# Kernel optimization log

Hardware: AMD Instinct MI355X
Metric: run time of the kernel (lower is better)

The kernel has to match this reference:

```python
import jax, jax.numpy as jnp
import numpy as np

N = 100000        # nodes
E = 1600000       # edges (avg degree 16)
F = 128           # num_features
H = 8             # heads
D = F // H        # head_dim


def setup_inputs() -> dict:
    key = jax.random.key(0)
    ks = jax.random.split(key, 11)
    s = 1.0 / np.sqrt(F)
    return {
        "feat": jax.random.normal(ks[0], (N, F), dtype=jnp.float32),
        "edge_src": jax.random.randint(ks[1], (E,), 0, N, dtype=jnp.int32),
        "edge_dst": jax.random.randint(ks[2], (E,), 0, N, dtype=jnp.int32),
        "Wq": jax.random.uniform(ks[3], (F, F), jnp.float32, -s, s),
        "bq": jax.random.uniform(ks[4], (F,), jnp.float32, -s, s),
        "Wk": jax.random.uniform(ks[5], (F, F), jnp.float32, -s, s),
        "bk": jax.random.uniform(ks[6], (F,), jnp.float32, -s, s),
        "Wv": jax.random.uniform(ks[7], (F, F), jnp.float32, -s, s),
        "bv": jax.random.uniform(ks[8], (F,), jnp.float32, -s, s),
        "Wo": jax.random.uniform(ks[9], (F, F), jnp.float32, -s, s),
        "bo": jax.random.uniform(ks[10], (F,), jnp.float32, -s, s),
    }


def reference(feat, edge_src, edge_dst, Wq, bq, Wk, bk, Wv, bv, Wo, bo):
    scale = D ** -0.5
    # projections, split into heads: [N, H, D]
    q = ((feat @ Wq.T + bq) * scale).reshape(N, H, D)
    k = (feat @ Wk.T + bk).reshape(N, H, D)
    v = (feat @ Wv.T + bv).reshape(N, H, D)

    # per-edge dot product k[src] . q[dst] -> [E, H]  (dfn.u_dot_v)
    scores = jnp.einsum('ehd,ehd->eh', k[edge_src], q[edge_dst])

    # edge softmax normalized over incoming edges of each dst node
    m = jax.ops.segment_max(scores, edge_dst, num_segments=N)  # [N, H]
    m = jnp.where(jnp.isfinite(m), m, 0.0)
    e = jnp.exp(scores - m[edge_dst])                          # [E, H]
    z = jax.ops.segment_sum(e, edge_dst, num_segments=N)       # [N, H]
    alpha = e / z[edge_dst]                                    # [E, H]

    # weighted sum aggregation (u_mul_e + sum): [N, H, D]
    wv = alpha[:, :, None] * v[edge_src]                       # [E, H, D]
    attn = jax.ops.segment_sum(wv, edge_dst, num_segments=N)

    return attn.reshape(N, F) @ Wo.T + bo
```

## Files before the change

kernel.cpp:

```cpp
#include <hip/hip_runtime.h>
#include <math.h>

#define N_NODES 100000
#define N_EDGES 1600000
#define FDIM 128
#define NHEAD 8
#define HDIM 16
#define SCAT_PHASES 4

using bf16x8 = __attribute__((ext_vector_type(8))) short;
using half8  = __attribute__((ext_vector_type(8))) _Float16;
using half2t = __attribute__((ext_vector_type(2))) _Float16;
using f32x4  = __attribute__((ext_vector_type(4))) float;
using f32x2  = __attribute__((ext_vector_type(2))) float;

__device__ inline unsigned short f2bf(float f) {
    union { float f; unsigned int u; } x; x.f = f;
    unsigned int u = x.u;
    return (unsigned short)((u + 0x7fffu + ((u >> 16) & 1u)) >> 16);
}
__device__ inline unsigned short f2h(float f) {
    _Float16 h = (_Float16)f;
    return __builtin_bit_cast(unsigned short, h);
}
__device__ inline unsigned int packh2(float a, float b) {
    return (unsigned int)f2h(a) | ((unsigned int)f2h(b) << 16);
}
__device__ inline float h_lo(unsigned int u) {
    return (float)__builtin_bit_cast(_Float16, (unsigned short)(u & 0xffffu));
}
__device__ inline float h_hi(unsigned int u) {
    return (float)__builtin_bit_cast(_Float16, (unsigned short)(u >> 16));
}

#if __has_builtin(__builtin_amdgcn_cvt_pk_fp8_f32)
__device__ inline unsigned char fp8_enc(float x) {
    return (unsigned char)(__builtin_amdgcn_cvt_pk_fp8_f32(x, x, 0, false) & 0xff);
}
#else
__device__ inline unsigned char fp8_enc(float x) {
    unsigned int u = __builtin_bit_cast(unsigned int, x);
    unsigned int s = (u >> 24) & 0x80;
    float ax = fabsf(x);
    if (!(ax >= 0.001953125f)) {
        int m = (int)(ax * 512.f + 0.5f);
        return (unsigned char)(s | (unsigned)(m > 7 ? 7 : m));
    }
    if (ax > 448.f) return (unsigned char)(s | 0x7e);
    int e; float fr = frexpf(ax, &e);
    int q = (int)(fr * 16.f + 0.5f);
    if (q == 16) { q = 8; e += 1; }
    int exp = e - 1 + 7;
    if (exp <= 0) { int m = (int)(ax * 512.f + 0.5f); return (unsigned char)(s | (unsigned)(m > 7 ? 7 : m)); }
    if (exp > 15) return (unsigned char)(s | 0x7e);
    return (unsigned char)(s | (exp << 3) | (q & 7));
}
#endif

#if __has_builtin(__builtin_amdgcn_cvt_pk_f32_fp8)
#define FP8_HW_DECODE 1
#else
__device__ inline float fp8_dec_sw(unsigned char b) {
    int s = b >> 7, e = (b >> 3) & 15, m = b & 7;
    float v = (e == 0) ? ldexpf((float)m, -9) : ldexpf((float)(8 + m), e - 10);
    return s ? -v : v;
}
#endif

__device__ inline float dot_fp8_16(uint4 kr, const float* __restrict__ qq) {
    float s = 0.f;
#ifdef FP8_HW_DECODE
    f32x2 p;
    p = __builtin_amdgcn_cvt_pk_f32_fp8(kr.x, false); s = fmaf(p[0], qq[0],  s); s = fmaf(p[1], qq[1],  s);
    p = __builtin_amdgcn_cvt_pk_f32_fp8(kr.x, true);  s = fmaf(p[0], qq[2],  s); s = fmaf(p[1], qq[3],  s);
    p = __builtin_amdgcn_cvt_pk_f32_fp8(kr.y, false); s = fmaf(p[0], qq[4],  s); s = fmaf(p[1], qq[5],  s);
    p = __builtin_amdgcn_cvt_pk_f32_fp8(kr.y, true);  s = fmaf(p[0], qq[6],  s); s = fmaf(p[1], qq[7],  s);
    p = __builtin_amdgcn_cvt_pk_f32_fp8(kr.z, false); s = fmaf(p[0], qq[8],  s); s = fmaf(p[1], qq[9],  s);
    p = __builtin_amdgcn_cvt_pk_f32_fp8(kr.z, true);  s = fmaf(p[0], qq[10], s); s = fmaf(p[1], qq[11], s);
    p = __builtin_amdgcn_cvt_pk_f32_fp8(kr.w, false); s = fmaf(p[0], qq[12], s); s = fmaf(p[1], qq[13], s);
    p = __builtin_amdgcn_cvt_pk_f32_fp8(kr.w, true);  s = fmaf(p[0], qq[14], s); s = fmaf(p[1], qq[15], s);
#else
    unsigned int wds[4] = {kr.x, kr.y, kr.z, kr.w};
#pragma unroll
    for (int i = 0; i < 4; ++i)
#pragma unroll
        for (int j = 0; j < 4; ++j)
            s = fmaf(fp8_dec_sw((wds[i] >> (8 * j)) & 0xff), qq[i * 4 + j], s);
#endif
    return s;
}

__global__ __launch_bounds__(256) void convert_w_kernel(
    const float* __restrict__ W0, const float* __restrict__ W1,
    const float* __restrict__ W2, const float* __restrict__ W3,
    unsigned short* __restrict__ out)
{
    int i = blockIdx.x * 256 + threadIdx.x;
    int j  = i & 7;
    int l  = (i >> 3) & 63;
    int fk = i >> 9;
    int ks = fk & 3, nf = fk >> 2;
    int s = (nf * 16 + (l & 15)) * FDIM + ks * 32 + (l >> 4) * 8 + j;
    out[i]             = f2bf(W0[s]);
    out[16384 + i]     = f2bf(W1[s]);
    out[2 * 16384 + i] = f2bf(W2[s]);
    out[3 * 16384 + i] = f2h(W3[s]);
}

struct GemmArgs {
    const unsigned short* W[3];
    const float* b[3];
    void* out[3];
    float scale[3];
};

template<int NP, bool IN_F32, bool MFMA_F16, int OUTM>
__global__ __launch_bounds__(256, 2) void mfma_gemm_v2(
    const void* __restrict__ Ain, GemmArgs ga, int nrows)
{
    __shared__ unsigned short A_s[128][136];
    __shared__ unsigned short W_sh[8192];

    const int t  = threadIdx.x;
    const int r0 = blockIdx.x * 128;

#pragma unroll
    for (int it = 0; it < 8; ++it) {
        int i = t + it * 256;
        int r = i >> 4, c8 = (i & 15) << 3;
        int gr = r0 + r;
        if (IN_F32) {
            float4 v0 = make_float4(0.f, 0.f, 0.f, 0.f), v1 = v0;
            if (gr < nrows) {
                const float* Af = (const float*)Ain;
                v0 = *(const float4*)&Af[(size_t)gr * FDIM + c8];
                v1 = *(const float4*)&Af[(size_t)gr * FDIM + c8 + 4];
            }
            uint4 pk;
            pk.x = (unsigned)f2bf(v0.x) | ((unsigned)f2bf(v0.y) << 16);
            pk.y = (unsigned)f2bf(v0.z) | ((unsigned)f2bf(v0.w) << 16);
            pk.z = (unsigned)f2bf(v1.x) | ((unsigned)f2bf(v1.y) << 16);
            pk.w = (unsigned)f2bf(v1.z) | ((unsigned)f2bf(v1.w) << 16);
            *(uint4*)&A_s[r][c8] = pk;
        } else {
            uint4 v = make_uint4(0u, 0u, 0u, 0u);
            if (gr < nrows) {
                const unsigned short* Ab = (const unsigned short*)Ain;
                v = *(const uint4*)&Ab[(size_t)gr * FDIM + c8];
            }
            *(uint4*)&A_s[r][c8] = v;
        }
    }
    __syncthreads();

    const int w  = t >> 6, l = t & 63;
    const int lr = l & 15, lk = l >> 4;

    bf16x8 a[2][4];
#pragma unroll
    for (int rg = 0; rg < 2; ++rg)
#pragma unroll
        for (int ks = 0; ks < 4; ++ks)
            a[rg][ks] = *(const bf16x8*)&A_s[w * 32 + rg * 16 + lr][ks * 32 + lk * 8];

#pragma unroll
    for (int p = 0; p < NP; ++p) {
        const unsigned short* Wsrc = ga.W[p];
        f32x4 acc[2][8];
#pragma unroll
        for (int rg = 0; rg < 2; ++rg)
#pragma unroll
            for (int nf = 0; nf < 8; ++nf) acc[rg][nf] = (f32x4){0.f, 0.f, 0.f, 0.f};

#pragma unroll
        for (int h = 0; h < 2; ++h) {
#pragma unroll
            for (int it = 0; it < 4; ++it) {
                int chunk = t + it * 256;
                *(uint4*)&W_sh[chunk * 8] = *(const uint4*)&Wsrc[h * 8192 + chunk * 8];
            }
            __syncthreads();
#pragma unroll
            for (int nfl = 0; nfl < 4; ++nfl) {
                int nf = h * 4 + nfl;
#pragma unroll
                for (int ks = 0; ks < 4; ++ks) {
                    bf16x8 bfr = *(const bf16x8*)&W_sh[((nfl * 4 + ks) * 64 + l) * 8];
                    if (MFMA_F16) {
                        acc[0][nf] = __builtin_amdgcn_mfma_f32_16x16x32_f16(
                            __builtin_bit_cast(half8, a[0][ks]), __builtin_bit_cast(half8, bfr),
                            acc[0][nf], 0, 0, 0);
                        acc[1][nf] = __builtin_amdgcn_mfma_f32_16x16x32_f16(
                            __builtin_bit_cast(half8, a[1][ks]), __builtin_bit_cast(half8, bfr),
                            acc[1][nf], 0, 0, 0);
                    } else {
                        acc[0][nf] = __builtin_amdgcn_mfma_f32_16x16x32_bf16(a[0][ks], bfr, acc[0][nf], 0, 0, 0);
                        acc[1][nf] = __builtin_amdgcn_mfma_f32_16x16x32_bf16(a[1][ks], bfr, acc[1][nf], 0, 0, 0);
                    }
                }
            }
            __syncthreads();
        }

        const float* bias = ga.b[p];
        const float  scl  = ga.scale[p];
        const int    mode = (OUTM >> (2 * p)) & 3;

        if (mode == 0) {
            unsigned short* Oh = &A_s[0][0];
#pragma unroll
            for (int rg = 0; rg < 2; ++rg)
#pragma unroll
                for (int nf = 0; nf < 8; ++nf) {
                    int col = nf * 16 + lr;
                    float bv = bias[col];
#pragma unroll
                    for (int j = 0; j < 4; ++j)
                        Oh[(w * 32 + rg * 16 + lk * 4 + j) * 136 + col] = f2h((acc[rg][nf][j] + bv) * scl);
                }
            __syncthreads();
            unsigned short* outp = (unsigned short*)ga.out[p];
#pragma unroll
            for (int it = 0; it < 8; ++it) {
                int i = t + it * 256;
                int r = i >> 4, c8 = (i & 15) << 3;
                if (r0 + r < nrows)
                    *(uint4*)&outp[(size_t)(r0 + r) * FDIM + c8] = *(const uint4*)&Oh[r * 136 + c8];
            }
        } else if (mode == 1) {
            unsigned char* O8 = (unsigned char*)A_s;
#pragma unroll
            for (int rg = 0; rg < 2; ++rg)
#pragma unroll
                for (int nf = 0; nf < 8; ++nf) {
                    int col = nf * 16 + lr;
                    float bv = bias[col];
#pragma unroll
                    for (int j = 0; j < 4; ++j)
                        O8[(w * 32 + rg * 16 + lk * 4 + j) * 144 + col] = fp8_enc((acc[rg][nf][j] + bv) * scl);
                }
            __syncthreads();
            unsigned char* outp = (unsigned char*)ga.out[p];
#pragma unroll
            for (int it = 0; it < 4; ++it) {
                int i = t + it * 256;
                int r = i >> 3, c16 = (i & 7) << 4;
                if (r0 + r < nrows)
                    *(uint4*)&outp[(size_t)(r0 + r) * FDIM + c16] = *(const uint4*)&O8[r * 144 + c16];
            }
        } else {
            float* outp = (float*)ga.out[p];
#pragma unroll
            for (int rg = 0; rg < 2; ++rg)
#pragma unroll
                for (int nf = 0; nf < 8; ++nf) {
                    int col = nf * 16 + lr;
                    float bv = bias[col];
                    int row = r0 + w * 32 + rg * 16 + lk * 4;
#pragma unroll
                    for (int j = 0; j < 4; ++j)
                        if (row + j < nrows)
                            outp[(size_t)(row + j) * FDIM + col] = (acc[rg][nf][j] + bv) * scl;
                }
        }
    }
}

__global__ void count_rank_kernel(const int* __restrict__ dst, int* __restrict__ cnt,
                                  unsigned short* __restrict__ rank, int n)
{
    int i = blockIdx.x * 256 + threadIdx.x;
    if (i < n) {
        int d = __builtin_nontemporal_load(&dst[i]);
        rank[i] = (unsigned short)atomicAdd(&cnt[d], 1);
    }
}

__global__ void scan_a_kernel(const int* __restrict__ cnt, int* __restrict__ row_off,
                              int* __restrict__ part, int n)
{
    __shared__ int s[256];
    int t = threadIdx.x;
    int gid = blockIdx.x * 256 + t;
    int x = (gid < n) ? cnt[gid] : 0;
    s[t] = x;
    __syncthreads();
    for (int off = 1; off < 256; off <<= 1) {
        int val = (t >= off) ? s[t - off] : 0;
        __syncthreads();
        s[t] += val;
        __syncthreads();
    }
    if (gid < n) row_off[gid] = s[t] - x;
    if (t == 255) part[blockIdx.x] = s[255];
}

__global__ void scan_b_kernel(int* __restrict__ part, int nb)
{
    __shared__ int s[512];
    int t = threadIdx.x;
    int x = (t < nb) ? part[t] : 0;
    s[t] = x;
    __syncthreads();
    for (int off = 1; off < 512; off <<= 1) {
        int val = (t >= off) ? s[t - off] : 0;
        __syncthreads();
        s[t] += val;
        __syncthreads();
    }
    if (t < nb) part[t] = s[t] - x;
}

__global__ void scan_c_kernel(int* __restrict__ row_off, const int* __restrict__ part,
                              int n, int total)
{
    int gid = blockIdx.x * 256 + threadIdx.x;
    if (gid < n) row_off[gid] += part[blockIdx.x];
    if (gid == 0) row_off[n] = total;
}

__global__ void scatter_phase_kernel(const int* __restrict__ src, const int* __restrict__ dst,
                                     const unsigned short* __restrict__ rank,
                                     const int* __restrict__ row_off,
                                     int* __restrict__ csr_src, int n, int lo, int hi)
{
    int i = blockIdx.x * 256 + threadIdx.x;
    if (i < n) {
        int d = __builtin_nontemporal_load(&dst[i]);
        if (d >= lo && d < hi) {
            int pos = row_off[d] + (int)__builtin_nontemporal_load(&rank[i]);
            csr_src[pos] = __builtin_nontemporal_load(&src[i]);
        }
    }
}

__global__ __launch_bounds__(256) void attn_kernel(
    const unsigned short* __restrict__ q, const unsigned char* __restrict__ kf8,
    const unsigned short* __restrict__ v,
    const int* __restrict__ row_off, const int* __restrict__ csr_src,
    unsigned short* __restrict__ out, int nnodes)
{
    __shared__ float q_s[4][NHEAD][18];
    __shared__ float sc_s[4][64][NHEAD];
    __shared__ int   src_s[4][64];

    const int w = threadIdx.x >> 6;
    const int l = threadIdx.x & 63;
    const int node = blockIdx.x * 4 + w;
    if (node >= nnodes) return;

    {
        unsigned int qv = *(const unsigned int*)&q[(size_t)node * FDIM + l * 2];
        q_s[w][l >> 3][(l & 7) * 2]     = h_lo(qv);
        q_s[w][l >> 3][(l & 7) * 2 + 1] = h_hi(qv);
    }

    const int e_l  = l >> 3, h_sc = l & 7;
    const int h_ag = l >> 3, dp   = l & 7;
    const int vo   = h_ag * HDIM + dp * 2;

    const int start = row_off[node];
    const int end   = row_off[node + 1];

    float  m_run = -INFINITY;
    float  z_run = 0.f;
    float2 acc   = make_float2(0.f, 0.f);

    for (int c0 = start; c0 < end; c0 += 64) {
        const int cn = min(64, end - c0);

        for (int i = l; i < cn; i += 64)
            src_s[w][i] = csr_src[c0 + i];

        float cm = -INFINITY;
        const float* qq = &q_s[w][h_sc][0];
        for (int base = 0; base < cn; base += 32) {
            uint4 kr[4];
#pragma unroll
            for (int it = 0; it < 4; ++it) {
                int ei = base + it * 8 + e_l;
                if (ei < cn)
                    kr[it] = *(const uint4*)&kf8[(size_t)src_s[w][ei] * FDIM + h_sc * 16];
            }
#pragma unroll
            for (int it = 0; it < 4; ++it) {
                int ei = base + it * 8 + e_l;
                if (ei < cn) {
                    float s = dot_fp8_16(kr[it], qq);
                    sc_s[w][ei][h_sc] = s;
                    cm = fmaxf(cm, s);
                }
            }
        }
#pragma unroll
        for (int mask = 8; mask < 64; mask <<= 1)
            cm = fmaxf(cm, __shfl_xor(cm, mask, 64));

        float m_new = fmaxf(m_run, cm);
        float scale = __expf(m_run - m_new);
        m_run = m_new;

        float zp = 0.f;
        for (int eb = 0; eb < cn; eb += 8) {
            int ei = eb + e_l;
            if (ei < cn) {
                float p = __expf(sc_s[w][ei][h_sc] - m_new);
                sc_s[w][ei][h_sc] = p;
                zp += p;
            }
        }
#pragma unroll
        for (int mask = 8; mask < 64; mask <<= 1)
            zp += __shfl_xor(zp, mask, 64);
        z_run = z_run * scale + zp;

        float sc_ag = __shfl(scale, h_ag, 64);
        acc.x *= sc_ag;
        acc.y *= sc_ag;
        int e = 0;
        for (; e + 4 <= cn; e += 4) {
            unsigned int v0 = *(const unsigned int*)&v[(size_t)src_s[w][e]     * FDIM + vo];
            unsigned int v1 = *(const unsigned int*)&v[(size_t)src_s[w][e + 1] * FDIM + vo];
            unsigned int v2 = *(const unsigned int*)&v[(size_t)src_s[w][e + 2] * FDIM + vo];
            unsigned int v3 = *(const unsigned int*)&v[(size_t)src_s[w][e + 3] * FDIM + vo];
            float p0 = sc_s[w][e][h_ag],     p1 = sc_s[w][e + 1][h_ag];
            float p2 = sc_s[w][e + 2][h_ag], p3 = sc_s[w][e + 3][h_ag];
            acc.x = fmaf(p0, h_lo(v0), acc.x); acc.y = fmaf(p0, h_hi(v0), acc.y);
            acc.x = fmaf(p1, h_lo(v1), acc.x); acc.y = fmaf(p1, h_hi(v1), acc.y);
            acc.x = fmaf(p2, h_lo(v2), acc.x); acc.y = fmaf(p2, h_hi(v2), acc.y);
            acc.x = fmaf(p3, h_lo(v3), acc.x); acc.y = fmaf(p3, h_hi(v3), acc.y);
        }
        for (; e < cn; ++e) {
            float p = sc_s[w][e][h_ag];
            unsigned int vv = *(const unsigned int*)&v[(size_t)src_s[w][e] * FDIM + vo];
            acc.x = fmaf(p, h_lo(vv), acc.x);
            acc.y = fmaf(p, h_hi(vv), acc.y);
        }
    }

    float z_ag = __shfl(z_run, h_ag, 64);
    float2 o = make_float2(0.f, 0.f);
    if (end > start) { o.x = acc.x / z_ag; o.y = acc.y / z_ag; }
    *(unsigned int*)&out[(size_t)node * FDIM + vo] = packh2(o.x, o.y);
}

extern "C" void kernel_launch(void* const* d_in, const int* in_sizes, int n_in,
                              void* d_out, int out_size, void* d_ws, size_t ws_size,
                              hipStream_t stream)
{
    const float* feat = (const float*)d_in[0];
    const int*   esrc = (const int*)d_in[1];
    const int*   edst = (const int*)d_in[2];
    const float* Wq   = (const float*)d_in[3];
    const float* bq   = (const float*)d_in[4];
    const float* Wk   = (const float*)d_in[5];
    const float* bk   = (const float*)d_in[6];
    const float* Wv   = (const float*)d_in[7];
    const float* bv   = (const float*)d_in[8];
    const float* Wo   = (const float*)d_in[9];
    const float* bo   = (const float*)d_in[10];
    float* out = (float*)d_out;

    const size_t NROW = (size_t)N_NODES * FDIM;
    unsigned short* qb  = (unsigned short*)d_ws;
    unsigned short* vb  = qb + NROW;
    unsigned short* ab  = vb + NROW;
    unsigned char*  kf8 = (unsigned char*)(ab + NROW);
    unsigned short* wbf = (unsigned short*)(kf8 + NROW);
    unsigned short* rank = wbf + 4 * 16384;
    int* cnt     = (int*)(rank + N_EDGES);
    int* row_off = cnt + N_NODES;
    int* part    = row_off + N_NODES + 1;
    int* csr_src = part + 512;

    const int gemmGrid = (N_NODES + 127) / 128;
    const int edgeGrid = (N_EDGES + 255) / 256;
    const int nb       = (N_NODES + 255) / 256;

    hipLaunchKernelGGL(convert_w_kernel, dim3(64), dim3(256), 0, stream,
                       Wq, Wk, Wv, Wo, wbf);

    GemmArgs qkv;
    qkv.W[0] = wbf;          qkv.b[0] = bq; qkv.out[0] = qb;  qkv.scale[0] = 0.25f;
    qkv.W[1] = wbf + 16384;  qkv.b[1] = bk; qkv.out[1] = kf8; qkv.scale[1] = 1.0f;
    qkv.W[2] = wbf + 32768;  qkv.b[2] = bv; qkv.out[2] = vb;  qkv.scale[2] = 1.0f;
    hipLaunchKernelGGL((mfma_gemm_v2<3, true, false, 4>), dim3(gemmGrid), dim3(256), 0, stream,
                       feat, qkv, N_NODES);

    hipMemsetAsync(cnt, 0, sizeof(int) * N_NODES, stream);
    hipLaunchKernelGGL(count_rank_kernel, dim3(edgeGrid), dim3(256), 0, stream,
                       edst, cnt, rank, N_EDGES);
    hipLaunchKernelGGL(scan_a_kernel, dim3(nb), dim3(256), 0, stream, cnt, row_off, part, N_NODES);
    hipLaunchKernelGGL(scan_b_kernel, dim3(1), dim3(512), 0, stream, part, nb);
    hipLaunchKernelGGL(scan_c_kernel, dim3(nb), dim3(256), 0, stream, row_off, part, N_NODES, N_EDGES);
    for (int ph = 0; ph < SCAT_PHASES; ++ph) {
        int lo = (int)((long long)N_NODES * ph / SCAT_PHASES);
        int hi = (int)((long long)N_NODES * (ph + 1) / SCAT_PHASES);
        hipLaunchKernelGGL(scatter_phase_kernel, dim3(edgeGrid), dim3(256), 0, stream,
                           esrc, edst, rank, row_off, csr_src, N_EDGES, lo, hi);
    }

    hipLaunchKernelGGL(attn_kernel, dim3((N_NODES + 3) / 4), dim3(256), 0, stream,
                       qb, kf8, vb, row_off, csr_src, ab, N_NODES);

    GemmArgs oprj;
    oprj.W[0] = wbf + 3 * 16384; oprj.b[0] = bo; oprj.out[0] = out; oprj.scale[0] = 1.0f;
    hipLaunchKernelGGL((mfma_gemm_v2<1, false, true, 2>), dim3(gemmGrid), dim3(256), 0, stream,
                       ab, oprj, N_NODES);
}
```

Baseline: 276.7 us.

## Drop softmax max-subtraction, fold log2e into q scale, widen V gather per lane

The attention kernel no longer tracks a running max. It folds log2(e) into the q projection scale and computes scores directly as exp2 of the dot product, which removes the max reduction, the rescaling, and the second exp pass over shared memory. The aggregation loop is reorganised so each lane loads 16-byte V vectors covering 8 dims for 4 edges at once, followed by a cross-lane reduction at the end. The dot product uses packed f32x2 math. Dropping the max subtraction risks overflow for large scores and relies on the scores staying bounded.

```diff
diff --git a/kernel.cpp b/kernel.cpp
--- a/kernel.cpp
+++ b/kernel.cpp
@@ -31,6 +31,13 @@
 }
 __device__ inline float h_hi(unsigned int u) {
     return (float)__builtin_bit_cast(_Float16, (unsigned short)(u >> 16));
+}
+__device__ inline float exp2_fast(float x) {
+#if __has_builtin(__builtin_amdgcn_exp2f)
+    return __builtin_amdgcn_exp2f(x);
+#else
+    return __expf(x * 0.6931471805599453f);
+#endif
 }
 
 #if __has_builtin(__builtin_amdgcn_cvt_pk_fp8_f32)
@@ -67,27 +74,30 @@
 }
 #endif
 
-__device__ inline float dot_fp8_16(uint4 kr, const float* __restrict__ qq) {
+__device__ inline float dot_fp8_16(uint4 kr, const f32x2* __restrict__ qq2) {
+#ifdef FP8_HW_DECODE
+    f32x2 a = {0.f, 0.f};
+    f32x2 p;
+    p = __builtin_amdgcn_cvt_pk_f32_fp8(kr.x, false); a += p * qq2[0];
+    p = __builtin_amdgcn_cvt_pk_f32_fp8(kr.x, true);  a += p * qq2[1];
+    p = __builtin_amdgcn_cvt_pk_f32_fp8(kr.y, false); a += p * qq2[2];
+    p = __builtin_amdgcn_cvt_pk_f32_fp8(kr.y, true);  a += p * qq2[3];
+    p = __builtin_amdgcn_cvt_pk_f32_fp8(kr.z, false); a += p * qq2[4];
+    p = __builtin_amdgcn_cvt_pk_f32_fp8(kr.z, true);  a += p * qq2[5];
+    p = __builtin_amdgcn_cvt_pk_f32_fp8(kr.w, false); a += p * qq2[6];
+    p = __builtin_amdgcn_cvt_pk_f32_fp8(kr.w, true);  a += p * qq2[7];
+    return a[0] + a[1];
+#else
+    const float* qq = (const float*)qq2;
     float s = 0.f;
-#ifdef FP8_HW_DECODE
-    f32x2 p;
-    p = __builtin_amdgcn_cvt_pk_f32_fp8(kr.x, false); s = fmaf(p[0], qq[0],  s); s = fmaf(p[1], qq[1],  s);
-    p = __builtin_amdgcn_cvt_pk_f32_fp8(kr.x, true);  s = fmaf(p[0], qq[2],  s); s = fmaf(p[1], qq[3],  s);
-    p = __builtin_amdgcn_cvt_pk_f32_fp8(kr.y, false); s = fmaf(p[0], qq[4],  s); s = fmaf(p[1], qq[5],  s);
-    p = __builtin_amdgcn_cvt_pk_f32_fp8(kr.y, true);  s = fmaf(p[0], qq[6],  s); s = fmaf(p[1], qq[7],  s);
-    p = __builtin_amdgcn_cvt_pk_f32_fp8(kr.z, false); s = fmaf(p[0], qq[8],  s); s = fmaf(p[1], qq[9],  s);
-    p = __builtin_amdgcn_cvt_pk_f32_fp8(kr.z, true);  s = fmaf(p[0], qq[10], s); s = fmaf(p[1], qq[11], s);
-    p = __builtin_amdgcn_cvt_pk_f32_fp8(kr.w, false); s = fmaf(p[0], qq[12], s); s = fmaf(p[1], qq[13], s);
-    p = __builtin_amdgcn_cvt_pk_f32_fp8(kr.w, true);  s = fmaf(p[0], qq[14], s); s = fmaf(p[1], qq[15], s);
-#else
     unsigned int wds[4] = {kr.x, kr.y, kr.z, kr.w};
 #pragma unroll
     for (int i = 0; i < 4; ++i)
 #pragma unroll
         for (int j = 0; j < 4; ++j)
             s = fmaf(fp8_dec_sw((wds[i] >> (8 * j)) & 0xff), qq[i * 4 + j], s);
+    return s;
 #endif
-    return s;
 }
 
 __global__ __launch_bounds__(256) void convert_w_kernel(
@@ -341,7 +351,7 @@
     unsigned short* __restrict__ out, int nnodes)
 {
     __shared__ float q_s[4][NHEAD][18];
-    __shared__ float sc_s[4][64][NHEAD];
+    __shared__ float p_s[4][64][NHEAD];
     __shared__ int   src_s[4][64];
 
     const int w = threadIdx.x >> 6;
@@ -351,20 +361,20 @@
 
     {
         unsigned int qv = *(const unsigned int*)&q[(size_t)node * FDIM + l * 2];
-        q_s[w][l >> 3][(l & 7) * 2]     = h_lo(qv);
-        q_s[w][l >> 3][(l & 7) * 2 + 1] = h_hi(qv);
-    }
-
-    const int e_l  = l >> 3, h_sc = l & 7;
-    const int h_ag = l >> 3, dp   = l & 7;
-    const int vo   = h_ag * HDIM + dp * 2;
+        *(f32x2*)&q_s[w][l >> 3][(l & 7) * 2] = (f32x2){h_lo(qv), h_hi(qv)};
+    }
+
+    const int e_l = l >> 3, h_sc = l & 7;
+    const int e2 = l >> 4, h_ag = (l >> 1) & 7, dq = l & 1;
+    const int vo = h_ag * HDIM + dq * 8;
 
     const int start = row_off[node];
     const int end   = row_off[node + 1];
 
-    float  m_run = -INFINITY;
-    float  z_run = 0.f;
-    float2 acc   = make_float2(0.f, 0.f);
+    float z_run = 0.f;
+    f32x2 acc[4] = {{0.f,0.f},{0.f,0.f},{0.f,0.f},{0.f,0.f}};
+
+    const f32x2* qq2 = (const f32x2*)&q_s[w][h_sc][0];
 
     for (int c0 = start; c0 < end; c0 += 64) {
         const int cn = min(64, end - c0);
@@ -372,8 +382,6 @@
         for (int i = l; i < cn; i += 64)
             src_s[w][i] = csr_src[c0 + i];
 
-        float cm = -INFINITY;
-        const float* qq = &q_s[w][h_sc][0];
         for (int base = 0; base < cn; base += 32) {
             uint4 kr[4];
 #pragma unroll
@@ -386,62 +394,51 @@
             for (int it = 0; it < 4; ++it) {
                 int ei = base + it * 8 + e_l;
                 if (ei < cn) {
-                    float s = dot_fp8_16(kr[it], qq);
-                    sc_s[w][ei][h_sc] = s;
-                    cm = fmaxf(cm, s);
+                    float p = exp2_fast(dot_fp8_16(kr[it], qq2));
+                    p_s[w][ei][h_sc] = p;
+                    z_run += p;
                 }
             }
         }
-#pragma unroll
-        for (int mask = 8; mask < 64; mask <<= 1)
-            cm = fmaxf(cm, __shfl_xor(cm, mask, 64));
-
-        float m_new = fmaxf(m_run, cm);
-        float scale = __expf(m_run - m_new);
-        m_run = m_new;
-
-        float zp = 0.f;
-        for (int eb = 0; eb < cn; eb += 8) {
-            int ei = eb + e_l;
-            if (ei < cn) {
-                float p = __expf(sc_s[w][ei][h_sc] - m_new);
-                sc_s[w][ei][h_sc] = p;
-                zp += p;
-            }
-        }
-#pragma unroll
-        for (int mask = 8; mask < 64; mask <<= 1)
-            zp += __shfl_xor(zp, mask, 64);
-        z_run = z_run * scale + zp;
-
-        float sc_ag = __shfl(scale, h_ag, 64);
-        acc.x *= sc_ag;
-        acc.y *= sc_ag;
-        int e = 0;
-        for (; e + 4 <= cn; e += 4) {
-            unsigned int v0 = *(const unsigned int*)&v[(size_t)src_s[w][e]     * FDIM + vo];
-            unsigned int v1 = *(const unsigned int*)&v[(size_t)src_s[w][e + 1] * FDIM + vo];
-            unsigned int v2 = *(const unsigned int*)&v[(size_t)src_s[w][e + 2] * FDIM + vo];
-            unsigned int v3 = *(const unsigned int*)&v[(size_t)src_s[w][e + 3] * FDIM + vo];
-            float p0 = sc_s[w][e][h_ag],     p1 = sc_s[w][e + 1][h_ag];
-            float p2 = sc_s[w][e + 2][h_ag], p3 = sc_s[w][e + 3][h_ag];
-            acc.x = fmaf(p0, h_lo(v0), acc.x); acc.y = fmaf(p0, h_hi(v0), acc.y);
-            acc.x = fmaf(p1, h_lo(v1), acc.x); acc.y = fmaf(p1, h_hi(v1), acc.y);
-            acc.x = fmaf(p2, h_lo(v2), acc.x); acc.y = fmaf(p2, h_hi(v2), acc.y);
-            acc.x = fmaf(p3, h_lo(v3), acc.x); acc.y = fmaf(p3, h_hi(v3), acc.y);
-        }
-        for (; e < cn; ++e) {
-            float p = sc_s[w][e][h_ag];
-            unsigned int vv = *(const unsigned int*)&v[(size_t)src_s[w][e] * FDIM + vo];
-            acc.x = fmaf(p, h_lo(vv), acc.x);
-            acc.y = fmaf(p, h_hi(vv), acc.y);
-        }
-    }
+
+        for (int base = 0; base < cn; base += 4) {
+            int e  = base + e2;
+            int ec = min(e, cn - 1);
+            float p = (e < cn) ? p_s[w][e][h_ag] : 0.f;
+            uint4 vv = *(const uint4*)&v[(size_t)src_s[w][ec] * FDIM + vo];
+            f32x2 p2 = {p, p};
+            acc[0] += p2 * (f32x2){h_lo(vv.x), h_hi(vv.x)};
+            acc[1] += p2 * (f32x2){h_lo(vv.y), h_hi(vv.y)};
+            acc[2] += p2 * (f32x2){h_lo(vv.z), h_hi(vv.z)};
+            acc[3] += p2 * (f32x2){h_lo(vv.w), h_hi(vv.w)};
+        }
+    }
+
+#pragma unroll
+    for (int mask = 8; mask < 64; mask <<= 1)
+        z_run += __shfl_xor(z_run, mask, 64);
+
+#pragma unroll
+    for (int mask = 16; mask < 64; mask <<= 1)
+#pragma unroll
+        for (int i = 0; i < 4; ++i) {
+            acc[i][0] += __shfl_xor(acc[i][0], mask, 64);
+            acc[i][1] += __shfl_xor(acc[i][1], mask, 64);
+        }
 
     float z_ag = __shfl(z_run, h_ag, 64);
-    float2 o = make_float2(0.f, 0.f);
-    if (end > start) { o.x = acc.x / z_ag; o.y = acc.y / z_ag; }
-    *(unsigned int*)&out[(size_t)node * FDIM + vo] = packh2(o.x, o.y);
+
+    if (e2 == 0) {
+        uint4 o = make_uint4(0u, 0u, 0u, 0u);
+        if (end > start) {
+            float rz = 1.0f / z_ag;
+            o.x = packh2(acc[0][0] * rz, acc[0][1] * rz);
+            o.y = packh2(acc[1][0] * rz, acc[1][1] * rz);
+            o.z = packh2(acc[2][0] * rz, acc[2][1] * rz);
+            o.w = packh2(acc[3][0] * rz, acc[3][1] * rz);
+        }
+        *(uint4*)&out[(size_t)node * FDIM + vo] = o;
+    }
 }
 
 extern "C" void kernel_launch(void* const* d_in, const int* in_sizes, int n_in,
@@ -481,7 +478,7 @@
                        Wq, Wk, Wv, Wo, wbf);
 
     GemmArgs qkv;
-    qkv.W[0] = wbf;          qkv.b[0] = bq; qkv.out[0] = qb;  qkv.scale[0] = 0.25f;
+    qkv.W[0] = wbf;          qkv.b[0] = bq; qkv.out[0] = qb;  qkv.scale[0] = 0.25f * 1.4426950408889634f;
     qkv.W[1] = wbf + 16384;  qkv.b[1] = bk; qkv.out[1] = kf8; qkv.scale[1] = 1.0f;
     qkv.W[2] = wbf + 32768;  qkv.b[2] = bv; qkv.out[2] = vb;  qkv.scale[2] = 1.0f;
     hipLaunchKernelGGL((mfma_gemm_v2<3, true, false, 4>), dim3(gemmGrid), dim3(256), 0, stream,
```

Measured after the change: 276.2 us. No clear change (-0.2%).
